# Optimization experiments

Hardware: AMD Instinct MI355X
Metric: run time of the kernel (lower is better)

The kernel has to match this reference:

```python
import jax, jax.numpy as jnp
import numpy as np

B, N, D, H, C = 4, 1024, 768, 12, 3
Dh = D // H                      # 64
HID = int(D * 4.0 * (2.0 / 3.0)) # 2048 (SwiGLU hidden)
EPS = 1e-5


def layernorm(x, g, b):
    m = jnp.mean(x, axis=-1, keepdims=True)
    v = jnp.mean(jnp.square(x - m), axis=-1, keepdims=True)
    return (x - m) * jax.lax.rsqrt(v + EPS) * g + b


def setup_inputs() -> dict:
    key = jax.random.key(0)
    ks = jax.random.split(key, 8)
    x = jax.random.normal(ks[0], (B, N, D), jnp.float32)
    coords = jax.random.uniform(ks[1], (B, N, C), jnp.float32)
    qkv_w = jax.random.normal(ks[2], (3 * D, D), jnp.float32) * 0.02
    qkv_b = jnp.zeros((3 * D,), jnp.float32)
    rel_w = jax.random.normal(ks[3], (H, C), jnp.float32) * 0.1
    ln1_g = jnp.ones((D,), jnp.float32)
    ln1_b = jnp.zeros((D,), jnp.float32)
    ln2_g = jnp.ones((D,), jnp.float32)
    ln2_b = jnp.zeros((D,), jnp.float32)
    win_w = jax.random.normal(ks[4], (2 * HID, D), jnp.float32) * 0.02
    win_b = jnp.zeros((2 * HID,), jnp.float32)
    wout_w = jax.random.normal(ks[5], (D, HID), jnp.float32) * 0.02
    wout_b = jnp.zeros((D,), jnp.float32)
    return dict(x=x, coords=coords, ln1_g=ln1_g, ln1_b=ln1_b, qkv_w=qkv_w,
                qkv_b=qkv_b, rel_w=rel_w, ln2_g=ln2_g, ln2_b=ln2_b,
                win_w=win_w, win_b=win_b, wout_w=wout_w, wout_b=wout_b)


def reference(x, coords, ln1_g, ln1_b, qkv_w, qkv_b, rel_w, ln2_g, ln2_b,
              win_w, win_b, wout_w, wout_b):
    # --- PatchAttention on norm1(x) ---
    h = layernorm(x, ln1_g, ln1_b)
    qkv = h @ qkv_w.T + qkv_b                    # (B,N,3D)
    q, k, v = jnp.split(qkv, 3, axis=-1)

    def heads(t):  # (B,N,D) -> (B,H,N,Dh)
        return t.reshape(B, N, H, Dh).transpose(0, 2, 1, 3)

    qh, kh, vh = heads(q), heads(k), heads(v)
    scale = 1.0 / np.sqrt(Dh).astype(np.float32)
    scores = jnp.einsum('bhid,bhjd->bhij', qh, kh) * scale
    # coord bias: (coords_i - coords_j) . W_h  ==  p[b,h,i] - p[b,h,j]
    p = jnp.einsum('bnc,hc->bhn', coords, rel_w)  # (B,H,N)
    scores = scores + p[:, :, :, None] - p[:, :, None, :]
    attn = jax.nn.softmax(scores, axis=-1)
    o = jnp.einsum('bhij,bhjd->bhid', attn, vh)   # (B,H,N,Dh)
    o = o.transpose(0, 2, 1, 3).reshape(B, N, D)
    x = x + o

    # --- SwiGLU FFN on norm2(x) ---
    h2 = layernorm(x, ln2_g, ln2_b)
    uv = h2 @ win_w.T + win_b                     # (B,N,2*HID)
    u, g = jnp.split(uv, 2, axis=-1)
    act = jax.nn.silu(u) * g
    return x + act @ wout_w.T + wout_b
```

## Files before the change

### kernel.cpp

```cpp
#include <hip/hip_runtime.h>
#include <math.h>

typedef unsigned short u16;
typedef __bf16 bf16x8 __attribute__((ext_vector_type(8)));
typedef __bf16 bf16x4 __attribute__((ext_vector_type(4)));
typedef u16 u16x4 __attribute__((ext_vector_type(4)));
typedef float f32x4 __attribute__((ext_vector_type(4)));

#define NTOK 1024
#define DMODEL 768
#define NHEAD 12
#define LD3 2304
#define HIDDIM 2048

__device__ __forceinline__ float b2f(u16 u) {
  unsigned int t = ((unsigned int)u) << 16;
  float f;
  __builtin_memcpy(&f, &t, 4);
  return f;
}
__device__ __forceinline__ u16 f2b(float f) {
  unsigned int t;
  __builtin_memcpy(&t, &f, 4);
  t += 0x7fffu + ((t >> 16) & 1u);
  return (u16)(t >> 16);
}

__device__ __forceinline__ void gl_lds16(const u16* g, u16* l) {
  __builtin_amdgcn_global_load_lds(
      (__attribute__((address_space(1))) const unsigned int*)g,
      (__attribute__((address_space(3))) unsigned int*)l, 16, 0, 0);
}

__global__ __launch_bounds__(256) void signal_kernel(float* __restrict__ out,
                                                     int n, float c) {
  int i = blockIdx.x * 256 + threadIdx.x;
  if (i < n) out[i] = c;
}

__global__ __launch_bounds__(256) void detect_kernel(const u16* __restrict__ x,
                                                     int* __restrict__ flag) {
  __shared__ int cnt;
  if (threadIdx.x == 0) cnt = 0;
  __syncthreads();
  int bad = 0;
  for (int i = threadIdx.x; i < 4096; i += 256) {
    u16 v = x[2 * i];
    int e = (v >> 7) & 0xFF;
    if (e >= 0xC0) bad++;
  }
  atomicAdd(&cnt, bad);
  __syncthreads();
  if (threadIdx.x == 0) *flag = (cnt >= 64) ? 1 : 0;
}

struct CanonJobs {
  const void* s[13];
  u16* d[13];
  int n[13];
};

__global__ __launch_bounds__(256) void canon_kernel(CanonJobs jobs,
                                                    const int* __restrict__ flag) {
  int j = blockIdx.y;
  int n = jobs.n[j];
  const void* s = jobs.s[j];
  u16* d = jobs.d[j];
  bool isf32 = (*flag != 0);
  for (int i = blockIdx.x * 256 + threadIdx.x; i < n; i += gridDim.x * 256) {
    d[i] = isf32 ? f2b(((const float*)s)[i]) : ((const u16*)s)[i];
  }
}

__global__ __launch_bounds__(256) void ln_bf16_kernel(
    const u16* __restrict__ x, const u16* __restrict__ g,
    const u16* __restrict__ b, u16* __restrict__ out) {
  int row = blockIdx.x;
  int tid = threadIdx.x;
  const u16* xr = x + (size_t)row * DMODEL;
  float v0 = b2f(xr[tid]), v1 = b2f(xr[tid + 256]), v2 = b2f(xr[tid + 512]);
  float s = v0 + v1 + v2;
  float q = v0 * v0 + v1 * v1 + v2 * v2;
#pragma unroll
  for (int off = 32; off; off >>= 1) {
    s += __shfl_xor(s, off, 64);
    q += __shfl_xor(q, off, 64);
  }
  __shared__ float rs[4], rq[4];
  int wv = tid >> 6;
  if ((tid & 63) == 0) { rs[wv] = s; rq[wv] = q; }
  __syncthreads();
  s = rs[0] + rs[1] + rs[2] + rs[3];
  q = rq[0] + rq[1] + rq[2] + rq[3];
  float mean = s * (1.0f / 768.0f);
  float var = q * (1.0f / 768.0f) - mean * mean;
  float inv = rsqrtf(var + 1e-5f);
  u16* outr = out + (size_t)row * DMODEL;
  outr[tid]       = f2b((v0 - mean) * inv * b2f(g[tid])       + b2f(b[tid]));
  outr[tid + 256] = f2b((v1 - mean) * inv * b2f(g[tid + 256]) + b2f(b[tid + 256]));
  outr[tid + 512] = f2b((v2 - mean) * inv * b2f(g[tid + 512]) + b2f(b[tid + 512]));
}

__global__ __launch_bounds__(256) void ln_f32_kernel(
    const float* __restrict__ x, const u16* __restrict__ g,
    const u16* __restrict__ b, u16* __restrict__ out) {
  int row = blockIdx.x;
  int tid = threadIdx.x;
  const float* xr = x + (size_t)row * DMODEL;
  float v0 = xr[tid], v1 = xr[tid + 256], v2 = xr[tid + 512];
  float s = v0 + v1 + v2;
  float q = v0 * v0 + v1 * v1 + v2 * v2;
#pragma unroll
  for (int off = 32; off; off >>= 1) {
    s += __shfl_xor(s, off, 64);
    q += __shfl_xor(q, off, 64);
  }
  __shared__ float rs[4], rq[4];
  int wv = tid >> 6;
  if ((tid & 63) == 0) { rs[wv] = s; rq[wv] = q; }
  __syncthreads();
  s = rs[0] + rs[1] + rs[2] + rs[3];
  q = rq[0] + rq[1] + rq[2] + rq[3];
  float mean = s * (1.0f / 768.0f);
  float var = q * (1.0f / 768.0f) - mean * mean;
  float inv = rsqrtf(var + 1e-5f);
  u16* outr = out + (size_t)row * DMODEL;
  outr[tid]       = f2b((v0 - mean) * inv * b2f(g[tid])       + b2f(b[tid]));
  outr[tid + 256] = f2b((v1 - mean) * inv * b2f(g[tid + 256]) + b2f(b[tid + 256]));
  outr[tid + 512] = f2b((v2 - mean) * inv * b2f(g[tid + 512]) + b2f(b[tid + 512]));
}

__device__ __forceinline__ void gemm128_mainloop(
    const u16* __restrict__ A, const u16* __restrict__ W, int K,
    int mB0, int nB0, u16* Al, u16* Bl, f32x4 (&acc)[4][4]) {
  int lane = threadIdx.x & 63;
  int wv = threadIdx.x >> 6;
  int q16 = lane & 15, quad = lane >> 4;
  int mW = (wv >> 1) * 64, nW = (wv & 1) * 64;
  int srow = lane >> 2, scol = (lane & 3) * 8;
  for (int k0 = 0; k0 < K; k0 += 32) {
#pragma unroll
    for (int c = 0; c < 2; ++c) {
      int ch = wv * 2 + c;
      int r = ch * 16 + srow;
      gl_lds16(A + (size_t)(mB0 + r) * K + k0 + scol, Al + ch * 512);
      gl_lds16(W + (size_t)(nB0 + r) * K + k0 + scol, Bl + ch * 512);
    }
    __syncthreads();
    bf16x8 af[4], bfr[4];
#pragma unroll
    for (int si = 0; si < 4; ++si)
      af[si] = *(const bf16x8*)((const __bf16*)Al + (mW + si * 16 + q16) * 32 + quad * 8);
#pragma unroll
    for (int sj = 0; sj < 4; ++sj)
      bfr[sj] = *(const bf16x8*)((const __bf16*)Bl + (nW + sj * 16 + q16) * 32 + quad * 8);
#pragma unroll
    for (int si = 0; si < 4; ++si)
#pragma unroll
      for (int sj = 0; sj < 4; ++sj)
        acc[si][sj] = __builtin_amdgcn_mfma_f32_16x16x32_bf16(af[si], bfr[sj], acc[si][sj], 0, 0, 0);
    __syncthreads();
  }
}

__global__ __launch_bounds__(256) void gemm_bt(
    const u16* __restrict__ Ap, const u16* __restrict__ Wp,
    const u16* __restrict__ bias, u16* __restrict__ Cp, int Nn, int K) {
  __shared__ __align__(16) u16 Al[128 * 32], Bl[128 * 32];
  int lane = threadIdx.x & 63;
  int wv = threadIdx.x >> 6;
  int q16 = lane & 15, quad = lane >> 4;
  int mBase = blockIdx.y * 128 + (wv >> 1) * 64;
  int nBase = blockIdx.x * 128 + (wv & 1) * 64;
  f32x4 acc[4][4] = {};
  gemm128_mainloop(Ap, Wp, K, blockIdx.y * 128, blockIdx.x * 128, Al, Bl, acc);
#pragma unroll
  for (int si = 0; si < 4; ++si)
#pragma unroll
    for (int sj = 0; sj < 4; ++sj) {
      int col = nBase + sj * 16 + q16;
      float bcol = b2f(bias[col]);
#pragma unroll
      for (int r = 0; r < 4; ++r) {
        int rowi = mBase + si * 16 + quad * 4 + r;
        Cp[(size_t)rowi * Nn + col] = f2b(acc[si][sj][r] + bcol);
      }
    }
}

__global__ __launch_bounds__(256) void gemm_out_f32(
    const u16* __restrict__ Ap, const u16* __restrict__ Wp,
    const u16* __restrict__ bias, const float* __restrict__ res,
    float* __restrict__ Cp, int Nn, int K) {
  __shared__ __align__(16) u16 Al[128 * 32], Bl[128 * 32];
  int lane = threadIdx.x & 63;
  int wv = threadIdx.x >> 6;
  int q16 = lane & 15, quad = lane >> 4;
  int mBase = blockIdx.y * 128 + (wv >> 1) * 64;
  int nBase = blockIdx.x * 128 + (wv & 1) * 64;
  f32x4 acc[4][4] = {};
  gemm128_mainloop(Ap, Wp, K, blockIdx.y * 128, blockIdx.x * 128, Al, Bl, acc);
#pragma unroll
  for (int si = 0; si < 4; ++si)
#pragma unroll
    for (int sj = 0; sj < 4; ++sj) {
      int col = nBase + sj * 16 + q16;
      float bcol = b2f(bias[col]);
#pragma unroll
      for (int r = 0; r < 4; ++r) {
        int rowi = mBase + si * 16 + quad * 4 + r;
        Cp[(size_t)rowi * Nn + col] = acc[si][sj][r] + bcol + res[(size_t)rowi * Nn + col];
      }
    }
}

__global__ __launch_bounds__(256) void ffn_in_kernel(
    const u16* __restrict__ hp, const u16* __restrict__ Wp,
    const u16* __restrict__ bias, u16* __restrict__ actp) {
  __shared__ __align__(16) u16 Al[128 * 32], Bl[128 * 32];
  int lane = threadIdx.x & 63;
  int wv = threadIdx.x >> 6;
  int q16 = lane & 15, quad = lane >> 4;
  int mB0 = blockIdx.y * 128;
  int cB0 = blockIdx.x * 64;
  int mW = (wv >> 1) * 64;
  int cW = (wv & 1) * 32;
  int srow = lane >> 2, scol = (lane & 3) * 8;
  f32x4 au[4][2] = {}, ag[4][2] = {};
  for (int k0 = 0; k0 < DMODEL; k0 += 32) {
#pragma unroll
    for (int c = 0; c < 2; ++c) {
      int ch = wv * 2 + c;
      int r = ch * 16 + srow;
      gl_lds16(hp + (size_t)(mB0 + r) * DMODEL + k0 + scol, Al + ch * 512);
      int grow = (r < 64) ? (cB0 + r) : (HIDDIM + cB0 + r - 64);
      gl_lds16(Wp + (size_t)grow * DMODEL + k0 + scol, Bl + ch * 512);
    }
    __syncthreads();
    bf16x8 af[4], wu[2], wg[2];
#pragma unroll
    for (int si = 0; si < 4; ++si)
      af[si] = *(const bf16x8*)((const __bf16*)Al + (mW + si * 16 + q16) * 32 + quad * 8);
#pragma unroll
    for (int sj = 0; sj < 2; ++sj) {
      wu[sj] = *(const bf16x8*)((const __bf16*)Bl + (cW + sj * 16 + q16) * 32 + quad * 8);
      wg[sj] = *(const bf16x8*)((const __bf16*)Bl + (64 + cW + sj * 16 + q16) * 32 + quad * 8);
    }
#pragma unroll
    for (int si = 0; si < 4; ++si)
#pragma unroll
      for (int sj = 0; sj < 2; ++sj) {
        au[si][sj] = __builtin_amdgcn_mfma_f32_16x16x32_bf16(af[si], wu[sj], au[si][sj], 0, 0, 0);
        ag[si][sj] = __builtin_amdgcn_mfma_f32_16x16x32_bf16(af[si], wg[sj], ag[si][sj], 0, 0, 0);
      }
    __syncthreads();
  }
#pragma unroll
  for (int si = 0; si < 4; ++si)
#pragma unroll
    for (int sj = 0; sj < 2; ++sj) {
      int col = cB0 + cW + sj * 16 + q16;
      float bu = b2f(bias[col]);
      float bg = b2f(bias[HIDDIM + col]);
#pragma unroll
      for (int r = 0; r < 4; ++r) {
        int rowi = mB0 + mW + si * 16 + quad * 4 + r;
        float u = au[si][sj][r] + bu;
        float g = ag[si][sj][r] + bg;
        float s = u / (1.0f + __expf(-u));
        actp[(size_t)rowi * HIDDIM + col] = f2b(s * g);
      }
    }
}

__global__ __launch_bounds__(256) void p_kernel(
    const u16* __restrict__ coords, const u16* __restrict__ relw,
    float* __restrict__ p) {
  const float LOG2E = 1.4426950408889634f;
  int idx = blockIdx.x * 256 + threadIdx.x;
  float c0 = b2f(coords[idx * 3 + 0]);
  float c1 = b2f(coords[idx * 3 + 1]);
  float c2 = b2f(coords[idx * 3 + 2]);
  int b = idx >> 10, n = idx & 1023;
#pragma unroll
  for (int h = 0; h < NHEAD; ++h) {
    float w0 = b2f(relw[h * 3 + 0]), w1 = b2f(relw[h * 3 + 1]), w2 = b2f(relw[h * 3 + 2]);
    p[(size_t)(b * NHEAD + h) * NTOK + n] = (c0 * w0 + c1 * w1 + c2 * w2) * LOG2E;
  }
}

__global__ __launch_bounds__(256) void vt_kernel(const u16* __restrict__ qkvp,
                                                 u16* __restrict__ vtp) {
  int blk = blockIdx.x;
  int b = blk / 192;
  int rem = blk % 192;
  int h = rem >> 4;
  int nt = rem & 15;
  int wv = threadIdx.x >> 6;
  int d = threadIdx.x & 63;
  int n0 = nt * 64 + wv * 16;
  const u16* src = qkvp + ((size_t)(b * NTOK) + n0) * LD3 + 2 * DMODEL + h * 64 + d;
  u16* dst = vtp + ((size_t)((b * NHEAD + h) * 64 + d)) * NTOK + n0;
#pragma unroll
  for (int c = 0; c < 2; ++c) {
    u16 buf[8] __attribute__((aligned(16)));
#pragma unroll
    for (int i = 0; i < 8; ++i) buf[i] = src[(size_t)(c * 8 + i) * LD3];
    *(uint4*)(dst + c * 8) = *(const uint4*)buf;
  }
}

__global__ __launch_bounds__(256) void attn_kernel(
    const u16* __restrict__ qkvp, const u16* __restrict__ vtp,
    const float* __restrict__ p2, const u16* __restrict__ xp,
    float* __restrict__ x1) {
  const __bf16* qb = (const __bf16*)qkvp;
  __shared__ __align__(16) u16 Kl[2][32 * 64];
  __shared__ __align__(16) u16 Vl[2][64 * 32];
  __shared__ __align__(16) u16 Pl[4][16][40];
  int lane = threadIdx.x & 63;
  int wv = threadIdx.x >> 6;
  int blk = blockIdx.x;
  int b = blk / 192;
  int rem = blk % 192;
  int h = rem >> 4;
  int i0 = ((rem & 15) * 4 + wv) * 16;
  int q16 = lane & 15, quad = lane >> 4;

  const float scl2 = 0.125f * 1.4426950408889634f;

  const __bf16* qrow = qb + ((size_t)(b * NTOK) + i0 + q16) * LD3 + h * 64;
  bf16x8 bq0 = *(const bf16x8*)(qrow + quad * 8);
  bf16x8 bq1 = *(const bf16x8*)(qrow + 32 + quad * 8);

  const float* prow = p2 + (size_t)(b * NHEAD + h) * NTOK;

  int krw = wv * 8 + (lane >> 3);
  int ks  = (lane & 7) ^ (krw & 7);
  const u16* kg0 = qkvp + (size_t)(b * NTOK) * LD3 + DMODEL + h * 64 + ks * 8;
  int vrw = wv * 16 + (lane >> 2);
  int vs  = (lane & 3) ^ (vrw & 3);
  const u16* vg0 = vtp + ((size_t)((b * NHEAD + h) * 64 + vrw)) * NTOK + vs * 8;

  float mrun = -1e30f, lsum = 0.f;
  f32x4 accO[4] = {};

  gl_lds16(kg0 + (size_t)krw * LD3, &Kl[0][wv * 512]);
  gl_lds16(vg0, &Vl[0][wv * 512]);
  __syncthreads();

  int buf = 0;
  for (int t = 0; t < 32; ++t) {
    int j0 = t * 32;
    if (t < 31) {
      gl_lds16(kg0 + (size_t)(j0 + 32 + krw) * LD3, &Kl[buf ^ 1][wv * 512]);
      gl_lds16(vg0 + j0 + 32, &Vl[buf ^ 1][wv * 512]);
    }

    const __bf16* Kb = (const __bf16*)Kl[buf];
    int kx0 = (quad ^ (q16 & 7)) << 3;
    int kx1 = ((4 | quad) ^ (q16 & 7)) << 3;
    bf16x8 ka00 = *(const bf16x8*)(Kb + q16 * 64 + kx0);
    bf16x8 ka01 = *(const bf16x8*)(Kb + q16 * 64 + kx1);
    bf16x8 ka10 = *(const bf16x8*)(Kb + (16 + q16) * 64 + kx0);
    bf16x8 ka11 = *(const bf16x8*)(Kb + (16 + q16) * 64 + kx1);
    f32x4 st0 = {}, st1 = {};
    st0 = __builtin_amdgcn_mfma_f32_16x16x32_bf16(ka00, bq0, st0, 0, 0, 0);
    st0 = __builtin_amdgcn_mfma_f32_16x16x32_bf16(ka01, bq1, st0, 0, 0, 0);
    st1 = __builtin_amdgcn_mfma_f32_16x16x32_bf16(ka10, bq0, st1, 0, 0, 0);
    st1 = __builtin_amdgcn_mfma_f32_16x16x32_bf16(ka11, bq1, st1, 0, 0, 0);

    f32x4 pjl = *(const f32x4*)(prow + j0 + 4 * quad);
    f32x4 pjh = *(const f32x4*)(prow + j0 + 16 + 4 * quad);
    float sl[4], sh[4];
#pragma unroll
    for (int r = 0; r < 4; ++r) {
      sl[r] = st0[r] * scl2 - pjl[r];
      sh[r] = st1[r] * scl2 - pjh[r];
    }
    float lm = fmaxf(fmaxf(fmaxf(sl[0], sl[1]), fmaxf(sl[2], sl[3])),
                     fmaxf(fmaxf(sh[0], sh[1]), fmaxf(sh[2], sh[3])));
    lm = fmaxf(lm, __shfl_xor(lm, 16, 64));
    lm = fmaxf(lm, __shfl_xor(lm, 32, 64));
    float mn = fmaxf(mrun, lm);
    float alpha = exp2f(mrun - mn);
    mrun = mn;
    float pl[4], ph[4];
#pragma unroll
    for (int r = 0; r < 4; ++r) {
      pl[r] = exp2f(sl[r] - mn);
      ph[r] = exp2f(sh[r] - mn);
    }
    float ts = (pl[0] + pl[1]) + (pl[2] + pl[3]) +
               (ph[0] + ph[1]) + (ph[2] + ph[3]);
    ts += __shfl_xor(ts, 16, 64);
    ts += __shfl_xor(ts, 32, 64);
    lsum = lsum * alpha + ts;

    bf16x4 w0 = {(__bf16)pl[0], (__bf16)pl[1], (__bf16)pl[2], (__bf16)pl[3]};
    bf16x4 w1 = {(__bf16)ph[0], (__bf16)ph[1], (__bf16)ph[2], (__bf16)ph[3]};
    *(bf16x4*)(&Pl[wv][q16][4 * quad]) = w0;
    *(bf16x4*)(&Pl[wv][q16][16 + 4 * quad]) = w1;
    bf16x8 ap = *(const bf16x8*)(&Pl[wv][q16][quad * 8]);

    const __bf16* Vb = (const __bf16*)Vl[buf];
    int vx = (quad ^ (q16 & 3)) << 3;
#pragma unroll
    for (int ds = 0; ds < 4; ++ds) {
      bf16x8 av = *(const bf16x8*)(Vb + (ds * 16 + q16) * 32 + vx);
      f32x4 c = accO[ds];
#pragma unroll
      for (int r = 0; r < 4; ++r) c[r] *= alpha;
      accO[ds] = __builtin_amdgcn_mfma_f32_16x16x32_bf16(av, ap, c, 0, 0, 0);
    }

    __syncthreads();
    buf ^= 1;
  }

  float rl = 1.0f / lsum;
  size_t rowbase = ((size_t)(b * NTOK) + i0 + q16) * DMODEL + h * 64;
#pragma unroll
  for (int ds = 0; ds < 4; ++ds) {
    int d0 = ds * 16 + quad * 4;
    u16x4 xv = *(const u16x4*)(xp + rowbase + d0);
    f32x4 ov;
#pragma unroll
    for (int r = 0; r < 4; ++r) ov[r] = b2f(xv[r]) + accO[ds][r] * rl;
    *(f32x4*)(x1 + rowbase + d0) = ov;
  }
}

extern "C" void kernel_launch(void* const* d_in, const int* in_sizes, int n_in,
                              void* d_out, int out_size, void* d_ws, size_t ws_size,
                              hipStream_t stream) {
  static const int esz[13] = {3145728, 12288, 768, 768, 1769472, 2304, 36,
                              768, 768, 3145728, 4096, 1572864, 768};
  float sig = -1.f;
  if (n_in != 13) {
    sig = 6000.f + 100.f * (float)n_in;
  } else {
    for (int i = 0; i < 13; ++i)
      if (in_sizes[i] != esz[i]) { sig = 1000.f + 100.f * (float)i; break; }
  }
  if (sig < 0.f && ws_size < 57258496ULL) sig = 3000.f;
  if (sig < 0.f && out_size != 3145728) sig = 3100.f;
  if (sig >= 0.f) {
    signal_kernel<<<(out_size + 255) / 256, 256, 0, stream>>>((float*)d_out, out_size, sig);
    return;
  }

  char* ws = (char*)d_ws;
  int*  flag    = (int*)ws;
  u16*  cx      = (u16*)(ws + 256);
  u16*  cqkvw   = (u16*)(ws + 6291712);
  u16*  cwinw   = (u16*)(ws + 9830656);
  u16*  cwoutw  = (u16*)(ws + 16122112);
  u16*  ccoords = (u16*)(ws + 19267840);
  u16*  cln1g   = (u16*)(ws + 19292416);
  u16*  cln1b   = (u16*)(ws + 19293952);
  u16*  cqkvb   = (u16*)(ws + 19295488);
  u16*  crelw   = (u16*)(ws + 19300096);
  u16*  cln2g   = (u16*)(ws + 19300352);
  u16*  cln2b   = (u16*)(ws + 19301888);
  u16*  cwinb   = (u16*)(ws + 19303424);
  u16*  cwoutb  = (u16*)(ws + 19311616);
  u16*  h       = (u16*)(ws + 19313152);
  u16*  qkv     = (u16*)(ws + 25604608);
  float* pbuf   = (float*)(ws + 44478976);
  float* x1     = (float*)(ws + 44675584);
  u16*  act     = qkv;
  u16*  vt      = h;

  detect_kernel<<<1, 256, 0, stream>>>((const u16*)d_in[0], flag);

  CanonJobs jobs;
  u16* dsts[13] = {cx, ccoords, cln1g, cln1b, cqkvw, cqkvb, crelw,
                   cln2g, cln2b, cwinw, cwinb, cwoutw, cwoutb};
  for (int i = 0; i < 13; ++i) {
    jobs.s[i] = d_in[i];
    jobs.d[i] = dsts[i];
    jobs.n[i] = in_sizes[i];
  }
  canon_kernel<<<dim3(3072, 13), 256, 0, stream>>>(jobs, flag);

  ln_bf16_kernel<<<4096, 256, 0, stream>>>(cx, cln1g, cln1b, h);
  gemm_bt<<<dim3(18, 32), 256, 0, stream>>>(h, cqkvw, cqkvb, qkv, 2304, 768);
  p_kernel<<<16, 256, 0, stream>>>(ccoords, crelw, pbuf);
  vt_kernel<<<768, 256, 0, stream>>>(qkv, vt);
  attn_kernel<<<768, 256, 0, stream>>>(qkv, vt, pbuf, cx, x1);
  ln_f32_kernel<<<4096, 256, 0, stream>>>(x1, cln2g, cln2b, h);
  ffn_in_kernel<<<dim3(32, 32), 256, 0, stream>>>(h, cwinw, cwinb, act);
  gemm_out_f32<<<dim3(6, 32), 256, 0, stream>>>(act, cwoutw, cwoutb, x1, (float*)d_out, 768, 2048);
}
```

Baseline: 303.1 us.

## Split-K the FFN output GEMM with narrower tiles and a reduction pass

```diff
diff --git a/kernel.cpp b/kernel.cpp
--- a/kernel.cpp
+++ b/kernel.cpp
@@ -188,30 +188,73 @@
     }
 }
 
-__global__ __launch_bounds__(256) void gemm_out_f32(
+__global__ __launch_bounds__(256) void gemm_out_split(
     const u16* __restrict__ Ap, const u16* __restrict__ Wp,
     const u16* __restrict__ bias, const float* __restrict__ res,
-    float* __restrict__ Cp, int Nn, int K) {
-  __shared__ __align__(16) u16 Al[128 * 32], Bl[128 * 32];
+    float* __restrict__ part, float* __restrict__ out) {
+  __shared__ __align__(16) u16 Al[128 * 32], Bl[64 * 32];
   int lane = threadIdx.x & 63;
   int wv = threadIdx.x >> 6;
   int q16 = lane & 15, quad = lane >> 4;
-  int mBase = blockIdx.y * 128 + (wv >> 1) * 64;
-  int nBase = blockIdx.x * 128 + (wv & 1) * 64;
-  f32x4 acc[4][4] = {};
-  gemm128_mainloop(Ap, Wp, K, blockIdx.y * 128, blockIdx.x * 128, Al, Bl, acc);
+  int mB0 = blockIdx.y * 128;
+  int nB0 = blockIdx.x * 64;
+  int kz = blockIdx.z;
+  int kbase = kz * 1024;
+  int mW = (wv >> 1) * 64, nW = (wv & 1) * 32;
+  int srow = lane >> 2, scol = (lane & 3) * 8;
+  f32x4 acc[4][2] = {};
+  for (int k0 = 0; k0 < 1024; k0 += 32) {
+#pragma unroll
+    for (int c = 0; c < 2; ++c) {
+      int ch = wv * 2 + c;
+      int r = ch * 16 + srow;
+      gl_lds16(Ap + (size_t)(mB0 + r) * 2048 + kbase + k0 + scol, Al + ch * 512);
+    }
+    {
+      int r = wv * 16 + srow;
+      gl_lds16(Wp + (size_t)(nB0 + r) * 2048 + kbase + k0 + scol, Bl + wv * 512);
+    }
+    __syncthreads();
+    bf16x8 af[4], bfr[2];
+#pragma unroll
+    for (int si = 0; si < 4; ++si)
+      af[si] = *(const bf16x8*)((const __bf16*)Al + (mW + si * 16 + q16) * 32 + quad * 8);
+#pragma unroll
+    for (int sj = 0; sj < 2; ++sj)
+      bfr[sj] = *(const bf16x8*)((const __bf16*)Bl + (nW + sj * 16 + q16) * 32 + quad * 8);
+#pragma unroll
+    for (int si = 0; si < 4; ++si)
+#pragma unroll
+      for (int sj = 0; sj < 2; ++sj)
+        acc[si][sj] = __builtin_amdgcn_mfma_f32_16x16x32_bf16(af[si], bfr[sj], acc[si][sj], 0, 0, 0);
+    __syncthreads();
+  }
 #pragma unroll
   for (int si = 0; si < 4; ++si)
 #pragma unroll
-    for (int sj = 0; sj < 4; ++sj) {
-      int col = nBase + sj * 16 + q16;
-      float bcol = b2f(bias[col]);
+    for (int sj = 0; sj < 2; ++sj) {
+      int col = nB0 + nW + sj * 16 + q16;
 #pragma unroll
       for (int r = 0; r < 4; ++r) {
-        int rowi = mBase + si * 16 + quad * 4 + r;
-        Cp[(size_t)rowi * Nn + col] = acc[si][sj][r] + bcol + res[(size_t)rowi * Nn + col];
+        int rowi = mB0 + mW + si * 16 + quad * 4 + r;
+        size_t idx = (size_t)rowi * 768 + col;
+        if (kz == 0) {
+          part[idx] = acc[si][sj][r];
+        } else {
+          out[idx] = acc[si][sj][r] + b2f(bias[col]) + res[idx];
+        }
       }
     }
+}
+
+__global__ __launch_bounds__(256) void add_kernel(float* __restrict__ out,
+                                                  const float* __restrict__ part) {
+  int i = blockIdx.x * 256 + threadIdx.x;
+  f32x4 o = ((f32x4*)out)[i];
+  f32x4 p = ((const f32x4*)part)[i];
+#pragma unroll
+  for (int r = 0; r < 4; ++r) o[r] += p[r];
+  ((f32x4*)out)[i] = o;
 }
 
 __global__ __launch_bounds__(256) void ffn_in_kernel(
@@ -471,6 +514,7 @@
   float* x1     = (float*)(ws + 44675584);
   u16*  act     = qkv;
   u16*  vt      = h;
+  float* part   = (float*)(ws + 256);
 
   detect_kernel<<<1, 256, 0, stream>>>((const u16*)d_in[0], flag);
 
@@ -491,5 +535,7 @@
   attn_kernel<<<768, 256, 0, stream>>>(qkv, vt, pbuf, cx, x1);
   ln_f32_kernel<<<4096, 256, 0, stream>>>(x1, cln2g, cln2b, h);
   ffn_in_kernel<<<dim3(32, 32), 256, 0, stream>>>(h, cwinw, cwinb, act);
-  gemm_out_f32<<<dim3(6, 32), 256, 0, stream>>>(act, cwoutw, cwoutb, x1, (float*)d_out, 768, 2048);
-}
+  gemm_out_split<<<dim3(12, 32, 2), 256, 0, stream>>>(act, cwoutw, cwoutb, x1,
+                                                      part, (float*)d_out);
+  add_kernel<<<3072, 256, 0, stream>>>((float*)d_out, part);
+}
```

After: 293.3 us. 1.03x faster.
